# Performance work log

Measured on AMD Instinct MI355X. Metric: run time of the kernel, lower is better.

Reference implementation:

```python
import jax, jax.numpy as jnp
import numpy as np

B, T, D = 64, 2048, 1024
H1, H2 = 512, 32


def setup_inputs() -> dict:
    key = jax.random.key(0)
    k1, k2, k3, k4, k5, k6, k7, k8 = jax.random.split(key, 8)
    avf_out = jax.random.normal(k1, (B, T, D), dtype=jnp.float32)
    seq_len = jax.random.randint(k2, (B,), 16, T + 1)  # int, >=16 so k<=seq_len
    s1 = 1.0 / np.sqrt(D)
    s2 = 1.0 / np.sqrt(H1)
    s3 = 1.0 / np.sqrt(H2)
    W1 = jax.random.uniform(k3, (D, H1), jnp.float32, -s1, s1)
    b1 = jax.random.uniform(k4, (H1,), jnp.float32, -s1, s1)
    W2 = jax.random.uniform(k5, (H1, H2), jnp.float32, -s2, s2)
    b2 = jax.random.uniform(k6, (H2,), jnp.float32, -s2, s2)
    W3 = jax.random.uniform(k7, (H2,), jnp.float32, -s3, s3)
    b3 = jax.random.uniform(k8, (), jnp.float32, -s3, s3)
    return {"avf_out": avf_out, "seq_len": seq_len, "W1": W1, "b1": b1,
            "W2": W2, "b2": b2, "W3": W3, "b3": b3}


def reference(avf_out, seq_len, W1, b1, W2, b2, W3, b3):
    h = jax.nn.relu(jnp.einsum('btd,dh->bth', avf_out, W1) + b1)  # [B,T,512]
    h = jnp.einsum('bth,hk->btk', h, W2) + b2                      # [B,T,32]
    logits = jax.nn.sigmoid(jnp.einsum('btk,k->bt', h, W3) + b3)   # [B,T]
    Tn = logits.shape[1]
    max_k = Tn // 16 + 1
    pos = jnp.arange(Tn)
    masked = jnp.where(pos[None, :] < seq_len[:, None], logits, -jnp.inf)
    topv, _ = jax.lax.top_k(masked, max_k)                         # [B,max_k]
    ks = seq_len // 16 + 1                                         # per-sample k
    kmask = jnp.arange(max_k)[None, :] < ks[:, None]
    out = jnp.sum(jnp.where(kmask, topv, 0.0), axis=1) / ks.astype(logits.dtype)
    return out  # [B]
```

## Files before the change

### kernel.cpp

```cpp
#include <hip/hip_runtime.h>
#include <hip/hip_bf16.h>
#include <stdint.h>
#include <math.h>

#define T_SEQ 2048
#define D_IN  1024
#define H1_N  512

typedef short  short8  __attribute__((ext_vector_type(8)));
typedef __bf16 bf16x8  __attribute__((ext_vector_type(8)));
typedef float  floatx4 __attribute__((ext_vector_type(4)));

#if defined(__HIP_DEVICE_COMPILE__) && __has_builtin(__builtin_amdgcn_global_load_lds)
#define HAS_GLL 1
#endif

__device__ __forceinline__ short f2bf(float f) {
    union { float f; unsigned u; } v; v.f = f;
    unsigned r = v.u + 0x7fffu + ((v.u >> 16) & 1u);
    return (short)(r >> 16);
}

__global__ __launch_bounds__(256)
void prep_kernel(const float* __restrict__ W1, const float* __restrict__ W2,
                 const float* __restrict__ b2, const float* __restrict__ W3,
                 const float* __restrict__ b3, short* __restrict__ W1T,
                 float* __restrict__ weff, float* __restrict__ ceff) {
    const int t = threadIdx.x;
    if (blockIdx.x == 128) {
        for (int h = t; h < H1_N; h += 256) {
            float s = 0.f;
            for (int k = 0; k < 32; ++k) s += W2[h * 32 + k] * W3[k];
            weff[h] = s;
        }
        if (t == 0) {
            float s = 0.f;
            for (int k = 0; k < 32; ++k) s += b2[k] * W3[k];
            *ceff = s + b3[0];
        }
        return;
    }
    __shared__ float tile[64][65];
    const int dx = blockIdx.x >> 3;
    const int ny = blockIdx.x & 7;
    const int d0 = dx * 64, n0 = ny * 64;
#pragma unroll
    for (int i = 0; i < 16; ++i) {
        int e = i * 256 + t;
        int r = e >> 6, c = e & 63;
        tile[r][c] = W1[(size_t)(d0 + r) * H1_N + n0 + c];
    }
    __syncthreads();
#pragma unroll
    for (int i = 0; i < 8; ++i) {
        int o = i * 512 + t * 2;
        int rr = o >> 6, cc = o & 63;
        unsigned lo = (unsigned short)f2bf(tile[cc][rr]);
        unsigned hi = (unsigned short)f2bf(tile[cc + 1][rr]);
        *(unsigned*)&W1T[(size_t)(n0 + rr) * D_IN + d0 + cc] = lo | (hi << 16);
    }
}

__global__ __launch_bounds__(512, 2)
void gemm_kernel(const float* __restrict__ avf, const int* __restrict__ seq_len,
                 const float* __restrict__ b1, const short* __restrict__ W1T,
                 const float* __restrict__ weff, const float* __restrict__ ceff_p,
                 float* __restrict__ logits) {
    const int b  = blockIdx.y;
    const int t0 = blockIdx.x * 128;
    const int seq = seq_len[b];
    if (t0 >= seq) return;

    __shared__ short Bs[H1_N * 64];
    __shared__ short As[128 * 72];
    __shared__ float red[128];

    const int t   = threadIdx.x;
    const int w   = t >> 6;
    const int l   = t & 63;
    const int q   = l >> 4;
    const int m16 = l & 15;
    const int wn  = (w & 3) * 128;
    const int wm  = (w >> 2) * 64;

    if (t < 128) red[t] = 0.f;

    floatx4 acc[4][8];
#pragma unroll
    for (int i = 0; i < 4; ++i)
#pragma unroll
        for (int j = 0; j < 8; ++j) acc[i][j] = (floatx4){0.f, 0.f, 0.f, 0.f};

    const size_t arow = ((size_t)b * T_SEQ + t0) * D_IN;

    for (int k0 = 0; k0 < D_IN; k0 += 64) {
        __syncthreads();

#pragma unroll
        for (int i = 0; i < 8; ++i) {
            int s = w * 512 + i * 64 + l;
            int n = s >> 3;
            int c = (s & 7) ^ (n & 7);
            const short* gsrc = W1T + (size_t)n * D_IN + k0 + c * 8;
#ifdef HAS_GLL
            __builtin_amdgcn_global_load_lds(
                (const __attribute__((address_space(1))) unsigned int*)gsrc,
                (__attribute__((address_space(3))) unsigned int*)((char*)Bs + (w * 512 + i * 64) * 16),
                16, 0, 0);
#else
            *(short8*)((char*)Bs + (size_t)s * 16) = *(const short8*)gsrc;
#endif
        }

#pragma unroll
        for (int j = 0; j < 2; ++j) {
            int idx = j * 512 + t;
            int m = idx >> 3, c = idx & 7;
            if (t0 + m < seq) {
                const float* g = avf + arow + (size_t)m * D_IN + k0 + c * 8;
                float4 f0 = *(const float4*)g;
                float4 f1 = *(const float4*)(g + 4);
                short8 v;
                v[0] = f2bf(f0.x); v[1] = f2bf(f0.y); v[2] = f2bf(f0.z); v[3] = f2bf(f0.w);
                v[4] = f2bf(f1.x); v[5] = f2bf(f1.y); v[6] = f2bf(f1.z); v[7] = f2bf(f1.w);
                *(short8*)(&As[m * 72 + c * 8]) = v;
            }
        }
        __syncthreads();

#pragma unroll
        for (int kt = 0; kt < 2; ++kt) {
            short8 af[4], bfr[8];
#pragma unroll
            for (int mt = 0; mt < 4; ++mt)
                af[mt] = *(const short8*)(&As[(wm + mt * 16 + m16) * 72 + kt * 32 + q * 8]);
#pragma unroll
            for (int nt = 0; nt < 8; ++nt) {
                int n = wn + nt * 16 + m16;
                int c = (kt * 4 + q) ^ (n & 7);
                bfr[nt] = *(const short8*)((char*)Bs + (size_t)(n * 8 + c) * 16);
            }
#pragma unroll
            for (int mt = 0; mt < 4; ++mt)
#pragma unroll
                for (int nt = 0; nt < 8; ++nt)
                    acc[mt][nt] = __builtin_amdgcn_mfma_f32_16x16x32_bf16(
                        __builtin_bit_cast(bf16x8, af[mt]),
                        __builtin_bit_cast(bf16x8, bfr[nt]),
                        acc[mt][nt], 0, 0, 0);
        }
    }

    float bv[8], wv[8];
#pragma unroll
    for (int nt = 0; nt < 8; ++nt) {
        int col = wn + nt * 16 + m16;
        bv[nt] = b1[col];
        wv[nt] = weff[col];
    }
#pragma unroll
    for (int mt = 0; mt < 4; ++mt) {
#pragma unroll
        for (int r = 0; r < 4; ++r) {
            float p = 0.f;
#pragma unroll
            for (int nt = 0; nt < 8; ++nt) {
                float h = acc[mt][nt][r] + bv[nt];
                p += fmaxf(h, 0.f) * wv[nt];
            }
#pragma unroll
            for (int off = 1; off < 16; off <<= 1) p += __shfl_xor(p, off, 64);
            if (m16 == 0) atomicAdd(&red[wm + mt * 16 + q * 4 + r], p);
        }
    }
    __syncthreads();
    if (t < 128) {
        float x = red[t] + ceff_p[0];
        logits[(size_t)b * T_SEQ + t0 + t] = 1.f / (1.f + __expf(-x));
    }
}

__global__ __launch_bounds__(256)
void topk_kernel(const float* __restrict__ logits, const int* __restrict__ seq_len,
                 float* __restrict__ out) {
    __shared__ unsigned hist[256];
    __shared__ unsigned sufA[256], sufB[256];
    __shared__ unsigned sh_sel, sh_want;
    __shared__ float rs[4];
    __shared__ unsigned rc[4];

    const int b = blockIdx.x;
    const int t = threadIdx.x;
    const int seq = seq_len[b];
    const int ks = seq / 16 + 1;
    const float* lg = logits + (size_t)b * T_SEQ;

    float r[8];
#pragma unroll
    for (int j = 0; j < 8; ++j) {
        int i = j * 256 + t;
        r[j] = (i < seq) ? lg[i] : 0.0f;
    }

    unsigned prefix = 0;
    unsigned want = (unsigned)ks;
    for (int shift = 24; shift >= 0; shift -= 8) {
        const unsigned maskHi = (shift == 24) ? 0u : (0xFFFFFFFFu << (shift + 8));
        hist[t] = 0;
        __syncthreads();
#pragma unroll
        for (int j = 0; j < 8; ++j) {
            unsigned u = __float_as_uint(r[j]);
            if ((u & maskHi) == (prefix & maskHi))
                atomicAdd(&hist[(u >> shift) & 0xFF], 1u);
        }
        __syncthreads();
        sufA[t] = hist[t];
        __syncthreads();
        unsigned* src = sufA; unsigned* dst = sufB;
#pragma unroll
        for (int off = 1; off < 256; off <<= 1) {
            dst[t] = src[t] + ((t + off < 256) ? src[t + off] : 0u);
            __syncthreads();
            unsigned* tmp = src; src = dst; dst = tmp;
        }
        unsigned ge = src[t];
        unsigned ge_next = (t < 255) ? src[t + 1] : 0u;
        if (ge >= want && ge_next < want) {
            sh_sel = (unsigned)t;
            sh_want = want - ge_next;
        }
        __syncthreads();
        prefix |= sh_sel << shift;
        want = sh_want;
    }

    const float pivot = __uint_as_float(prefix);
    float s = 0.f; unsigned cgt = 0;
#pragma unroll
    for (int j = 0; j < 8; ++j) {
        float x = r[j];
        if (x > pivot) { s += x; cgt++; }
    }
#pragma unroll
    for (int off = 32; off > 0; off >>= 1) {
        s   += __shfl_down(s, off, 64);
        cgt += __shfl_down(cgt, off, 64);
    }
    if ((t & 63) == 0) { rs[t >> 6] = s; rc[t >> 6] = cgt; }
    __syncthreads();
    if (t == 0) {
        float S = rs[0] + rs[1] + rs[2] + rs[3];
        unsigned C = rc[0] + rc[1] + rc[2] + rc[3];
        out[b] = (S + (float)(ks - (int)C) * pivot) / (float)ks;
    }
}

extern "C" void kernel_launch(void* const* d_in, const int* in_sizes, int n_in,
                              void* d_out, int out_size, void* d_ws, size_t ws_size,
                              hipStream_t stream) {
    const float* avf = (const float*)d_in[0];
    const int*   seq = (const int*)  d_in[1];
    const float* W1  = (const float*)d_in[2];
    const float* b1  = (const float*)d_in[3];
    const float* W2  = (const float*)d_in[4];
    const float* b2  = (const float*)d_in[5];
    const float* W3  = (const float*)d_in[6];
    const float* b3  = (const float*)d_in[7];
    float* out = (float*)d_out;

    short* W1T    = (short*)d_ws;
    float* weff   = (float*)((char*)d_ws + (1 << 20));
    float* ceff   = weff + 512;
    float* logits = weff + 1024;

    prep_kernel<<<dim3(129), dim3(256), 0, stream>>>(W1, W2, b2, W3, b3, W1T, weff, ceff);
    gemm_kernel<<<dim3(T_SEQ / 128, 64), dim3(512), 0, stream>>>(avf, seq, b1, W1T, weff, ceff, logits);
    topk_kernel<<<dim3(64), dim3(256), 0, stream>>>(logits, seq, out);
}
```

Measured before the change: 811.8 us.

## Double-buffer W1 tiles in LDS and prefetch activation tiles into registers

Adds a second LDS buffer for the W1 tile and restructures the K loop as a software pipeline. The next W1 tile is issued into the alternate buffer and the next fp32 activation slice is loaded into registers before the current tile's MFMA work, then converted and written to LDS after a barrier. The goal is to hide global-memory latency behind the matrix math rather than stalling at the top of each iteration. In exchange, LDS use grows to about 146 KB per block, roughly 16 extra registers are held for the prefetch, and each iteration still has two barriers.

```diff
diff --git a/kernel.cpp b/kernel.cpp
--- a/kernel.cpp
+++ b/kernel.cpp
@@ -71,7 +71,7 @@
     const int seq = seq_len[b];
     if (t0 >= seq) return;
 
-    __shared__ short Bs[H1_N * 64];
+    __shared__ short Bs[2][H1_N * 64];
     __shared__ short As[128 * 72];
     __shared__ float red[128];
 
@@ -93,9 +93,14 @@
 
     const size_t arow = ((size_t)b * T_SEQ + t0) * D_IN;
 
-    for (int k0 = 0; k0 < D_IN; k0 += 64) {
-        __syncthreads();
-
+    const int am0 = t >> 3, ac0 = t & 7;
+    const int am1 = (512 + t) >> 3, ac1 = t & 7;
+    const bool alive0 = (t0 + am0 < seq);
+    const bool alive1 = (t0 + am1 < seq);
+
+    float4 apre[2][2];
+
+    auto stageB = [&](int k0, int nxt) {
 #pragma unroll
         for (int i = 0; i < 8; ++i) {
             int s = w * 512 + i * 64 + l;
@@ -105,28 +110,57 @@
 #ifdef HAS_GLL
             __builtin_amdgcn_global_load_lds(
                 (const __attribute__((address_space(1))) unsigned int*)gsrc,
-                (__attribute__((address_space(3))) unsigned int*)((char*)Bs + (w * 512 + i * 64) * 16),
+                (__attribute__((address_space(3))) unsigned int*)((char*)&Bs[nxt][0] + (w * 512 + i * 64) * 16),
                 16, 0, 0);
 #else
-            *(short8*)((char*)Bs + (size_t)s * 16) = *(const short8*)gsrc;
+            *(short8*)((char*)&Bs[nxt][0] + (size_t)s * 16) = *(const short8*)gsrc;
 #endif
         }
-
-#pragma unroll
-        for (int j = 0; j < 2; ++j) {
-            int idx = j * 512 + t;
-            int m = idx >> 3, c = idx & 7;
-            if (t0 + m < seq) {
-                const float* g = avf + arow + (size_t)m * D_IN + k0 + c * 8;
-                float4 f0 = *(const float4*)g;
-                float4 f1 = *(const float4*)(g + 4);
-                short8 v;
-                v[0] = f2bf(f0.x); v[1] = f2bf(f0.y); v[2] = f2bf(f0.z); v[3] = f2bf(f0.w);
-                v[4] = f2bf(f1.x); v[5] = f2bf(f1.y); v[6] = f2bf(f1.z); v[7] = f2bf(f1.w);
-                *(short8*)(&As[m * 72 + c * 8]) = v;
-            }
-        }
-        __syncthreads();
+    };
+
+    auto loadA = [&](int k0) {
+        if (alive0) {
+            const float* g = avf + arow + (size_t)am0 * D_IN + k0 + ac0 * 8;
+            apre[0][0] = *(const float4*)g;
+            apre[0][1] = *(const float4*)(g + 4);
+        }
+        if (alive1) {
+            const float* g = avf + arow + (size_t)am1 * D_IN + k0 + ac1 * 8;
+            apre[1][0] = *(const float4*)g;
+            apre[1][1] = *(const float4*)(g + 4);
+        }
+    };
+
+    auto writeA = [&]() {
+        if (alive0) {
+            short8 v;
+            v[0] = f2bf(apre[0][0].x); v[1] = f2bf(apre[0][0].y);
+            v[2] = f2bf(apre[0][0].z); v[3] = f2bf(apre[0][0].w);
+            v[4] = f2bf(apre[0][1].x); v[5] = f2bf(apre[0][1].y);
+            v[6] = f2bf(apre[0][1].z); v[7] = f2bf(apre[0][1].w);
+            *(short8*)(&As[am0 * 72 + ac0 * 8]) = v;
+        }
+        if (alive1) {
+            short8 v;
+            v[0] = f2bf(apre[1][0].x); v[1] = f2bf(apre[1][0].y);
+            v[2] = f2bf(apre[1][0].z); v[3] = f2bf(apre[1][0].w);
+            v[4] = f2bf(apre[1][1].x); v[5] = f2bf(apre[1][1].y);
+            v[6] = f2bf(apre[1][1].z); v[7] = f2bf(apre[1][1].w);
+            *(short8*)(&As[am1 * 72 + ac1 * 8]) = v;
+        }
+    };
+
+    stageB(0, 0);
+    loadA(0);
+    writeA();
+    __syncthreads();
+
+    int cur = 0;
+    for (int it = 0; it < 16; ++it) {
+        if (it < 15) {
+            stageB((it + 1) * 64, cur ^ 1);
+            loadA((it + 1) * 64);
+        }
 
 #pragma unroll
         for (int kt = 0; kt < 2; ++kt) {
@@ -138,7 +172,7 @@
             for (int nt = 0; nt < 8; ++nt) {
                 int n = wn + nt * 16 + m16;
                 int c = (kt * 4 + q) ^ (n & 7);
-                bfr[nt] = *(const short8*)((char*)Bs + (size_t)(n * 8 + c) * 16);
+                bfr[nt] = *(const short8*)((char*)&Bs[cur][0] + (size_t)(n * 8 + c) * 16);
             }
 #pragma unroll
             for (int mt = 0; mt < 4; ++mt)
@@ -149,6 +183,11 @@
                         __builtin_bit_cast(bf16x8, bfr[nt]),
                         acc[mt][nt], 0, 0, 0);
         }
+
+        __syncthreads();
+        if (it < 15) writeA();
+        __syncthreads();
+        cur ^= 1;
     }
 
     float bv[8], wv[8];
```

Result: faster. 772.5 us (-4.8%).

## Double-buffer GEMM tiles with A prefetch and fuse top-k via last-block counter

Applied to the files above, without the earlier changes.

The GEMM main loop now double-buffers the W1T tile in LDS and prefetches activation rows into registers two k-steps ahead, using explicit waitcnt and barrier calls so that loads overlap with MFMA work. The separate top-k kernel is removed: each block bumps a per-sample atomic counter, and the last block for a sample runs the radix top-k selection, reusing the LDS buffer. This removes a kernel launch and hides global load latency. The cost is doubled B-tile LDS, which may lower occupancy, plus fragile hand-written wait counts.

```diff
diff --git a/kernel.cpp b/kernel.cpp
--- a/kernel.cpp
+++ b/kernel.cpp
@@ -25,7 +25,8 @@
 void prep_kernel(const float* __restrict__ W1, const float* __restrict__ W2,
                  const float* __restrict__ b2, const float* __restrict__ W3,
                  const float* __restrict__ b3, short* __restrict__ W1T,
-                 float* __restrict__ weff, float* __restrict__ ceff) {
+                 float* __restrict__ weff, float* __restrict__ ceff,
+                 unsigned* __restrict__ ctr) {
     const int t = threadIdx.x;
     if (blockIdx.x == 128) {
         for (int h = t; h < H1_N; h += 256) {
@@ -33,6 +34,7 @@
             for (int k = 0; k < 32; ++k) s += W2[h * 32 + k] * W3[k];
             weff[h] = s;
         }
+        if (t < 64) ctr[t] = 0u;
         if (t == 0) {
             float s = 0.f;
             for (int k = 0; k < 32; ++k) s += b2[k] * W3[k];
@@ -61,19 +63,27 @@
     }
 }
 
+#define BARRIER_   do { __builtin_amdgcn_s_barrier(); __builtin_amdgcn_sched_barrier(0); } while (0)
+#define WAITLGKM0_ do { asm volatile("s_waitcnt lgkmcnt(0)" ::: "memory"); __builtin_amdgcn_sched_barrier(0); } while (0)
+#define WAITVM4_   do { asm volatile("s_waitcnt vmcnt(4)"   ::: "memory"); __builtin_amdgcn_sched_barrier(0); } while (0)
+#define WAITVM0_   do { asm volatile("s_waitcnt vmcnt(0)"   ::: "memory"); __builtin_amdgcn_sched_barrier(0); } while (0)
+
 __global__ __launch_bounds__(512, 2)
 void gemm_kernel(const float* __restrict__ avf, const int* __restrict__ seq_len,
                  const float* __restrict__ b1, const short* __restrict__ W1T,
                  const float* __restrict__ weff, const float* __restrict__ ceff_p,
-                 float* __restrict__ logits) {
+                 float* __restrict__ logits, unsigned* __restrict__ ctr,
+                 float* __restrict__ out) {
     const int b  = blockIdx.y;
     const int t0 = blockIdx.x * 128;
     const int seq = seq_len[b];
     if (t0 >= seq) return;
 
-    __shared__ short Bs[H1_N * 64];
+    __shared__ short Bs[2][H1_N * 64];
     __shared__ short As[128 * 72];
     __shared__ float red[128];
+    __shared__ int   sflag;
+    __shared__ unsigned sh_sel, sh_want;
 
     const int t   = threadIdx.x;
     const int w   = t >> 6;
@@ -91,11 +101,16 @@
 #pragma unroll
         for (int j = 0; j < 8; ++j) acc[i][j] = (floatx4){0.f, 0.f, 0.f, 0.f};
 
-    const size_t arow = ((size_t)b * T_SEQ + t0) * D_IN;
-
-    for (int k0 = 0; k0 < D_IN; k0 += 64) {
-        __syncthreads();
-
+    const int am0 = t >> 3, ac0 = t & 7;
+    const int am1 = 64 + (t >> 3), ac1 = t & 7;
+    int gr0 = t0 + am0; if (gr0 >= seq) gr0 = seq - 1;
+    int gr1 = t0 + am1; if (gr1 >= seq) gr1 = seq - 1;
+    const float* aptr0 = avf + ((size_t)b * T_SEQ + gr0) * D_IN + ac0 * 8;
+    const float* aptr1 = avf + ((size_t)b * T_SEQ + gr1) * D_IN + ac1 * 8;
+
+    float4 apreA[2][2], apreB[2][2];
+
+    auto stageB = [&](int k0, int nxt) {
 #pragma unroll
         for (int i = 0; i < 8; ++i) {
             int s = w * 512 + i * 64 + l;
@@ -105,29 +120,40 @@
 #ifdef HAS_GLL
             __builtin_amdgcn_global_load_lds(
                 (const __attribute__((address_space(1))) unsigned int*)gsrc,
-                (__attribute__((address_space(3))) unsigned int*)((char*)Bs + (w * 512 + i * 64) * 16),
+                (__attribute__((address_space(3))) unsigned int*)((char*)&Bs[nxt][0] + (w * 512 + i * 64) * 16),
                 16, 0, 0);
 #else
-            *(short8*)((char*)Bs + (size_t)s * 16) = *(const short8*)gsrc;
+            *(short8*)((char*)&Bs[nxt][0] + (size_t)s * 16) = *(const short8*)gsrc;
 #endif
         }
-
-#pragma unroll
-        for (int j = 0; j < 2; ++j) {
-            int idx = j * 512 + t;
-            int m = idx >> 3, c = idx & 7;
-            if (t0 + m < seq) {
-                const float* g = avf + arow + (size_t)m * D_IN + k0 + c * 8;
-                float4 f0 = *(const float4*)g;
-                float4 f1 = *(const float4*)(g + 4);
-                short8 v;
-                v[0] = f2bf(f0.x); v[1] = f2bf(f0.y); v[2] = f2bf(f0.z); v[3] = f2bf(f0.w);
-                v[4] = f2bf(f1.x); v[5] = f2bf(f1.y); v[6] = f2bf(f1.z); v[7] = f2bf(f1.w);
-                *(short8*)(&As[m * 72 + c * 8]) = v;
-            }
-        }
-        __syncthreads();
-
+        __builtin_amdgcn_sched_barrier(0);
+    };
+
+#define LOADA(K0, APRE) do {                                                  \
+        const float* _g0 = aptr0 + (K0);                                      \
+        (APRE)[0][0] = *(const float4*)_g0;                                   \
+        (APRE)[0][1] = *(const float4*)(_g0 + 4);                             \
+        const float* _g1 = aptr1 + (K0);                                      \
+        (APRE)[1][0] = *(const float4*)_g1;                                   \
+        (APRE)[1][1] = *(const float4*)(_g1 + 4);                             \
+    } while (0)
+
+#define WRITEA(APRE) do {                                                     \
+        short8 _v;                                                            \
+        _v[0] = f2bf((APRE)[0][0].x); _v[1] = f2bf((APRE)[0][0].y);           \
+        _v[2] = f2bf((APRE)[0][0].z); _v[3] = f2bf((APRE)[0][0].w);           \
+        _v[4] = f2bf((APRE)[0][1].x); _v[5] = f2bf((APRE)[0][1].y);           \
+        _v[6] = f2bf((APRE)[0][1].z); _v[7] = f2bf((APRE)[0][1].w);           \
+        *(short8*)(&As[am0 * 72 + ac0 * 8]) = _v;                             \
+        _v[0] = f2bf((APRE)[1][0].x); _v[1] = f2bf((APRE)[1][0].y);           \
+        _v[2] = f2bf((APRE)[1][0].z); _v[3] = f2bf((APRE)[1][0].w);           \
+        _v[4] = f2bf((APRE)[1][1].x); _v[5] = f2bf((APRE)[1][1].y);           \
+        _v[6] = f2bf((APRE)[1][1].z); _v[7] = f2bf((APRE)[1][1].w);           \
+        *(short8*)(&As[am1 * 72 + ac1 * 8]) = _v;                             \
+    } while (0)
+
+    int cur = 0;
+    auto computeTile = [&]() {
 #pragma unroll
         for (int kt = 0; kt < 2; ++kt) {
             short8 af[4], bfr[8];
@@ -138,7 +164,7 @@
             for (int nt = 0; nt < 8; ++nt) {
                 int n = wn + nt * 16 + m16;
                 int c = (kt * 4 + q) ^ (n & 7);
-                bfr[nt] = *(const short8*)((char*)Bs + (size_t)(n * 8 + c) * 16);
+                bfr[nt] = *(const short8*)((char*)&Bs[cur][0] + (size_t)(n * 8 + c) * 16);
             }
 #pragma unroll
             for (int mt = 0; mt < 4; ++mt)
@@ -149,7 +175,30 @@
                         __builtin_bit_cast(bf16x8, bfr[nt]),
                         acc[mt][nt], 0, 0, 0);
         }
-    }
+    };
+
+    stageB(0, 0);
+    LOADA(0, apreA);
+    LOADA(64, apreB);
+    WRITEA(apreA);
+    WAITLGKM0_;
+    BARRIER_;
+
+#define GITER(IT, APRE) do {                                                  \
+        if ((IT) > 0) { WRITEA(APRE); WAITLGKM0_; BARRIER_; }                 \
+        if ((IT) < 15) stageB(((IT) + 1) * 64, cur ^ 1);                      \
+        if ((IT) < 14) LOADA(((IT) + 2) * 64, APRE);                          \
+        computeTile();                                                        \
+        if ((IT) < 14)       { WAITVM4_; BARRIER_; }                          \
+        else if ((IT) == 14) { WAITVM0_; BARRIER_; }                          \
+        cur ^= 1;                                                             \
+    } while (0)
+
+    for (int itt = 0; itt < 8; ++itt) {
+        GITER(2 * itt,     apreA);
+        GITER(2 * itt + 1, apreB);
+    }
+#undef GITER
 
     float bv[8], wv[8];
 #pragma unroll
@@ -178,57 +227,62 @@
         float x = red[t] + ceff_p[0];
         logits[(size_t)b * T_SEQ + t0 + t] = 1.f / (1.f + __expf(-x));
     }
-}
-
-__global__ __launch_bounds__(256)
-void topk_kernel(const float* __restrict__ logits, const int* __restrict__ seq_len,
-                 float* __restrict__ out) {
-    __shared__ unsigned hist[256];
-    __shared__ unsigned sufA[256], sufB[256];
-    __shared__ unsigned sh_sel, sh_want;
-    __shared__ float rs[4];
-    __shared__ unsigned rc[4];
-
-    const int b = blockIdx.x;
-    const int t = threadIdx.x;
-    const int seq = seq_len[b];
+
+    const int nlive = (seq + 127) >> 7;
+    __syncthreads();
+    if (t == 0) {
+        __threadfence();
+        unsigned prev = atomicAdd(&ctr[b], 1u);
+        sflag = (prev == (unsigned)(nlive - 1)) ? 1 : 0;
+    }
+    __syncthreads();
+    if (!sflag) return;
+    __threadfence();
+
+    unsigned* hist = (unsigned*)&Bs[0][0];
+    unsigned* sfA  = hist + 256;
+    unsigned* sfB  = sfA + 256;
+    float*    rs   = (float*)(sfB + 256);
+    unsigned* rc   = (unsigned*)(rs + 8);
+
     const int ks = seq / 16 + 1;
     const float* lg = logits + (size_t)b * T_SEQ;
-
-    float r[8];
-#pragma unroll
-    for (int j = 0; j < 8; ++j) {
-        int i = j * 256 + t;
-        r[j] = (i < seq) ? lg[i] : 0.0f;
+    float rv[4];
+#pragma unroll
+    for (int j = 0; j < 4; ++j) {
+        int i = j * 512 + t;
+        rv[j] = (i < seq) ? lg[i] : 0.0f;
     }
 
     unsigned prefix = 0;
     unsigned want = (unsigned)ks;
     for (int shift = 24; shift >= 0; shift -= 8) {
         const unsigned maskHi = (shift == 24) ? 0u : (0xFFFFFFFFu << (shift + 8));
-        hist[t] = 0;
+        if (t < 256) hist[t] = 0;
         __syncthreads();
 #pragma unroll
-        for (int j = 0; j < 8; ++j) {
-            unsigned u = __float_as_uint(r[j]);
+        for (int j = 0; j < 4; ++j) {
+            unsigned u = __float_as_uint(rv[j]);
             if ((u & maskHi) == (prefix & maskHi))
                 atomicAdd(&hist[(u >> shift) & 0xFF], 1u);
         }
         __syncthreads();
-        sufA[t] = hist[t];
+        if (t < 256) sfA[t] = hist[t];
         __syncthreads();
-        unsigned* src = sufA; unsigned* dst = sufB;
+        unsigned* src = sfA; unsigned* dst = sfB;
 #pragma unroll
         for (int off = 1; off < 256; off <<= 1) {
-            dst[t] = src[t] + ((t + off < 256) ? src[t + off] : 0u);
+            if (t < 256) dst[t] = src[t] + ((t + off < 256) ? src[t + off] : 0u);
             __syncthreads();
             unsigned* tmp = src; src = dst; dst = tmp;
         }
-        unsigned ge = src[t];
-        unsigned ge_next = (t < 255) ? src[t + 1] : 0u;
-        if (ge >= want && ge_next < want) {
-            sh_sel = (unsigned)t;
-            sh_want = want - ge_next;
+        if (t < 256) {
+            unsigned ge = src[t];
+            unsigned ge_next = (t < 255) ? src[t + 1] : 0u;
+            if (ge >= want && ge_next < want) {
+                sh_sel = (unsigned)t;
+                sh_want = want - ge_next;
+            }
         }
         __syncthreads();
         prefix |= sh_sel << shift;
@@ -238,8 +292,8 @@
     const float pivot = __uint_as_float(prefix);
     float s = 0.f; unsigned cgt = 0;
 #pragma unroll
-    for (int j = 0; j < 8; ++j) {
-        float x = r[j];
+    for (int j = 0; j < 4; ++j) {
+        float x = rv[j];
         if (x > pivot) { s += x; cgt++; }
     }
 #pragma unroll
@@ -247,13 +301,16 @@
         s   += __shfl_down(s, off, 64);
         cgt += __shfl_down(cgt, off, 64);
     }
-    if ((t & 63) == 0) { rs[t >> 6] = s; rc[t >> 6] = cgt; }
+    if (l == 0) { rs[w] = s; rc[w] = cgt; }
     __syncthreads();
     if (t == 0) {
-        float S = rs[0] + rs[1] + rs[2] + rs[3];
-        unsigned C = rc[0] + rc[1] + rc[2] + rc[3];
+        float S = 0.f; unsigned C = 0;
+#pragma unroll
+        for (int i = 0; i < 8; ++i) { S += rs[i]; C += rc[i]; }
         out[b] = (S + (float)(ks - (int)C) * pivot) / (float)ks;
     }
+#undef LOADA
+#undef WRITEA
 }
 
 extern "C" void kernel_launch(void* const* d_in, const int* in_sizes, int n_in,
@@ -269,12 +326,12 @@
     const float* b3  = (const float*)d_in[7];
     float* out = (float*)d_out;
 
-    short* W1T    = (short*)d_ws;
-    float* weff   = (float*)((char*)d_ws + (1 << 20));
-    float* ceff   = weff + 512;
-    float* logits = weff + 1024;
-
-    prep_kernel<<<dim3(129), dim3(256), 0, stream>>>(W1, W2, b2, W3, b3, W1T, weff, ceff);
-    gemm_kernel<<<dim3(T_SEQ / 128, 64), dim3(512), 0, stream>>>(avf, seq, b1, W1T, weff, ceff, logits);
-    topk_kernel<<<dim3(64), dim3(256), 0, stream>>>(logits, seq, out);
+    short* W1T      = (short*)d_ws;
+    float* weff     = (float*)((char*)d_ws + (1 << 20));
+    float* ceff     = weff + 512;
+    float* logits   = weff + 1024;
+    unsigned* ctr   = (unsigned*)(logits + 64 * T_SEQ);
+
+    prep_kernel<<<dim3(129), dim3(256), 0, stream>>>(W1, W2, b2, W3, b3, W1T, weff, ceff, ctr);
+    gemm_kernel<<<dim3(T_SEQ / 128, 64), dim3(512), 0, stream>>>(avf, seq, b1, W1T, weff, ceff, logits, ctr, out);
 }
```

New measurement: 1.048 ms. 29.1% more time.
